# Kernel tuning notes

Hardware: AMD Instinct MI355X
Metric: run time of the kernel (lower is better)

Reference implementation:

```python
import jax, jax.numpy as jnp
import numpy as np

R = 32768          # number of human-object pairs
IN_FEATS = 3072    # input_size * 3 (person + object + union features)
HIDDEN = 1024      # input_size
NUM_CLASSES = 50   # action classes


def setup_inputs() -> dict:
    key = jax.random.key(0)
    k_x, k_w1, k_w2 = jax.random.split(key, 3)
    x = jax.random.normal(k_x, (R, IN_FEATS), dtype=jnp.float32)
    # Linear weights init: normal(std=0.01), bias 0 (as in the module)
    w1 = jax.random.normal(k_w1, (IN_FEATS, HIDDEN), dtype=jnp.float32) * 0.01
    b1 = jnp.zeros((HIDDEN,), dtype=jnp.float32)
    w2 = jax.random.normal(k_w2, (HIDDEN, NUM_CLASSES), dtype=jnp.float32) * 0.01
    b2 = jnp.zeros((NUM_CLASSES,), dtype=jnp.float32)
    return {"x": x, "w1": w1, "b1": b1, "w2": w2, "b2": b2}


def reference(x, w1, b1, w2, b2):
    # HoiOutputLayers.forward: scores = cls_score(relu(cls_fc1(x)))
    h = jax.nn.relu(jnp.dot(x, w1) + b1)          # [R, HIDDEN]
    scores = jnp.dot(h, w2) + b2                  # [R, NUM_CLASSES] action logits
    return scores
```

## Files before the change

### kernel.cpp

```cpp
#include <hip/hip_runtime.h>

#define K1 3072
#define N1 1024
#define NCOL 50

typedef float  f32x4  __attribute__((ext_vector_type(4)));
typedef short  short8 __attribute__((ext_vector_type(8)));

#define GLD16(g, l)                                                        \
  __builtin_amdgcn_global_load_lds(                                        \
      (const __attribute__((address_space(1))) void*)(g),                  \
      (__attribute__((address_space(3))) void*)(l), 16, 0, 0)

#define MFMA_BF16(a, b, c) __builtin_amdgcn_mfma_f32_16x16x32_bf16(a, b, c, 0, 0, 0)

__device__ inline unsigned bfr(float f) {
  return (__builtin_bit_cast(unsigned, f) + 0x8000u) >> 16;
}
__device__ inline short f2bf(float f) { return (short)bfr(f); }
__device__ inline short8 cvt8(float4 a, float4 b) {
  short8 r;
  r[0] = f2bf(a.x); r[1] = f2bf(a.y); r[2] = f2bf(a.z); r[3] = f2bf(a.w);
  r[4] = f2bf(b.x); r[5] = f2bf(b.y); r[6] = f2bf(b.z); r[7] = f2bf(b.w);
  return r;
}

__global__ __launch_bounds__(256) void w1t_kernel(const float* __restrict__ W1,
                                                  short* __restrict__ W1T) {
  __shared__ float tile[64 * 65];
  const int t = threadIdx.x, b = blockIdx.x;
  const int k0 = (b >> 4) * 64, n0 = (b & 15) * 64;
#pragma unroll
  for (int i = 0; i < 16; ++i) {
    const int e = t + i * 256, r = e >> 6, c = e & 63;
    tile[r * 65 + c] = W1[(size_t)(k0 + r) * N1 + n0 + c];
  }
  __syncthreads();
#pragma unroll
  for (int i = 0; i < 16; ++i) {
    const int e = t + i * 256, kx = e & 63, ny = e >> 6;
    W1T[(size_t)(n0 + ny) * K1 + k0 + kx] = f2bf(tile[kx * 65 + ny]);
  }
}

__global__ __launch_bounds__(256) void w2t_kernel(const float* __restrict__ W2,
                                                  short* __restrict__ W2T) {
  const int idx = blockIdx.x * 256 + threadIdx.x;
  for (int e = idx; e < 64 * N1; e += 16 * 256) {
    const int c = e >> 10, k = e & 1023;
    const float v = (c < NCOL) ? W2[(size_t)k * NCOL + c] : 0.f;
    W2T[(size_t)c * N1 + k] = f2bf(v);
  }
}

#define BK2 64
#define NIT (K1 / BK2)
#define ASLOT (256 * 64)
#define SH2 264

struct __align__(16) Smem2 {
  union {
    struct { short A[2][ASLOT]; short B[2][ASLOT]; } s;
    struct { short h[128 * SH2]; short w2t[64 * SH2]; } e;
  } u;
};

__global__ __launch_bounds__(512, 2)
void hoi_fused2(const float* __restrict__ X, const short* __restrict__ W1T,
                const float* __restrict__ B1, const short* __restrict__ W2T,
                const float* __restrict__ B2, float* __restrict__ OUT) {
  __shared__ Smem2 sm;
  const int tid  = threadIdx.x;
  const int lane = tid & 63, wid = tid >> 6;
  const int wr = wid >> 2, wc = wid & 3;
  const int l15 = lane & 15, g = lane >> 4, l7 = l15 & 7;

  const int bid  = blockIdx.x;
  const int gidx = (bid & 7) * 64 + (bid >> 3);
  const int m_blk = gidx >> 2, n_blk = gidx & 3;
  const int m0 = m_blk * 256, n0 = n_blk * 256;

  const int ar = tid >> 1;
  const int ah = tid & 1;
  const float* aptr = X + (size_t)(m0 + ar) * K1 + ah * 32;
  const int awr = ar * 64;
  const int ar7 = ar & 7;

  const int srow  = lane >> 3;
  const int sslot = (lane & 7) ^ srow;
  const short* bS0 = W1T + (size_t)(n0 + 0   + wid * 16 + srow) * K1 + sslot * 8;
  const short* bS1 = W1T + (size_t)(n0 + 128 + wid * 16 + srow) * K1 + sslot * 8;
  const int dL0 = (0   + wid * 16) * 64;
  const int dL1 = (128 + wid * 16) * 64;

#define ISSUE_B0(kt, sl) do { GLD16(bS0 + (size_t)(kt) * BK2,                  &sm.u.s.B[sl][dL0]);        \
                              GLD16(bS0 + (size_t)8 * K1 + (size_t)(kt) * BK2, &sm.u.s.B[sl][dL0 + 512]); } while (0)
#define ISSUE_B1(kt, sl) do { GLD16(bS1 + (size_t)(kt) * BK2,                  &sm.u.s.B[sl][dL1]);        \
                              GLD16(bS1 + (size_t)8 * K1 + (size_t)(kt) * BK2, &sm.u.s.B[sl][dL1 + 512]); } while (0)

  const int aRd = (wr * 128 + l15) * 64;
  const int bRd = (wc * 64  + l15) * 64;
  const int sk0 = ((g)     ^ l7) * 8;
  const int sk1 = ((4 | g) ^ l7) * 8;

  float b1v[4];
#pragma unroll
  for (int nf = 0; nf < 4; ++nf) b1v[nf] = B1[n0 + wc * 64 + nf * 16 + l15];

  f32x4 acc[8][4] = {};
  float4 ra[8];

  ISSUE_B0(0, 0); ISSUE_B1(0, 0);
#pragma unroll
  for (int q = 0; q < 8; ++q) ra[q] = *(const float4*)(aptr + 4 * q);
#pragma unroll
  for (int j = 0; j < 4; ++j) {
    const short8 v = cvt8(ra[2 * j], ra[2 * j + 1]);
    *(short8*)&sm.u.s.A[0][awr + (((ah << 2) | j) ^ ar7) * 8] = v;
  }
#pragma unroll
  for (int q = 0; q < 8; ++q) ra[q] = *(const float4*)(aptr + BK2 + 4 * q);

  for (int t = 0; t < NIT; ++t) {
    const int s  = t & 1, sx = s ^ 1;
    const int tn = (t + 1 < NIT) ? t + 1 : NIT - 1;
    const int ta = (t + 2 < NIT) ? t + 2 : NIT - 1;

    asm volatile("s_waitcnt vmcnt(8)" ::: "memory");
    asm volatile("s_waitcnt lgkmcnt(0)" ::: "memory");
    __builtin_amdgcn_s_barrier();
    __builtin_amdgcn_sched_barrier(0);

    short8 a_[4][2], b_[4][2];

#pragma unroll
    for (int mf = 0; mf < 4; ++mf) {
      a_[mf][0] = *(const short8*)&sm.u.s.A[s][aRd + mf * 1024 + sk0];
      a_[mf][1] = *(const short8*)&sm.u.s.A[s][aRd + mf * 1024 + sk1];
    }
#pragma unroll
    for (int nf = 0; nf < 2; ++nf) {
      b_[nf][0] = *(const short8*)&sm.u.s.B[s][bRd + nf * 1024 + sk0];
      b_[nf][1] = *(const short8*)&sm.u.s.B[s][bRd + nf * 1024 + sk1];
    }
    asm volatile("s_waitcnt lgkmcnt(0)" ::: "memory");
    __builtin_amdgcn_sched_barrier(0);
    __builtin_amdgcn_s_setprio(1);
#pragma unroll
    for (int mf = 0; mf < 4; ++mf)
#pragma unroll
      for (int nf = 0; nf < 2; ++nf) {
        acc[mf][nf] = MFMA_BF16(a_[mf][0], b_[nf][0], acc[mf][nf]);
        acc[mf][nf] = MFMA_BF16(a_[mf][1], b_[nf][1], acc[mf][nf]);
      }
    __builtin_amdgcn_s_setprio(0);
    ISSUE_B0(tn, sx);
    __builtin_amdgcn_sched_barrier(0);

#pragma unroll
    for (int nf = 2; nf < 4; ++nf) {
      b_[nf][0] = *(const short8*)&sm.u.s.B[s][bRd + nf * 1024 + sk0];
      b_[nf][1] = *(const short8*)&sm.u.s.B[s][bRd + nf * 1024 + sk1];
    }
    asm volatile("s_waitcnt lgkmcnt(0)" ::: "memory");
    __builtin_amdgcn_sched_barrier(0);
    __builtin_amdgcn_s_setprio(1);
#pragma unroll
    for (int mf = 0; mf < 4; ++mf)
#pragma unroll
      for (int nf = 2; nf < 4; ++nf) {
        acc[mf][nf] = MFMA_BF16(a_[mf][0], b_[nf][0], acc[mf][nf]);
        acc[mf][nf] = MFMA_BF16(a_[mf][1], b_[nf][1], acc[mf][nf]);
      }
    __builtin_amdgcn_s_setprio(0);
    ISSUE_B1(tn, sx);
    __builtin_amdgcn_sched_barrier(0);

#pragma unroll
    for (int mf = 0; mf < 4; ++mf) {
      a_[mf][0] = *(const short8*)&sm.u.s.A[s][aRd + (4 + mf) * 1024 + sk0];
      a_[mf][1] = *(const short8*)&sm.u.s.A[s][aRd + (4 + mf) * 1024 + sk1];
    }
    asm volatile("s_waitcnt lgkmcnt(0)" ::: "memory");
    __builtin_amdgcn_sched_barrier(0);
    __builtin_amdgcn_s_setprio(1);
#pragma unroll
    for (int mf = 0; mf < 4; ++mf)
#pragma unroll
      for (int nf = 0; nf < 2; ++nf) {
        acc[4 + mf][nf] = MFMA_BF16(a_[mf][0], b_[nf][0], acc[4 + mf][nf]);
        acc[4 + mf][nf] = MFMA_BF16(a_[mf][1], b_[nf][1], acc[4 + mf][nf]);
      }
    __builtin_amdgcn_s_setprio(0);
#pragma unroll
    for (int j = 0; j < 4; ++j) {
      const short8 v = cvt8(ra[2 * j], ra[2 * j + 1]);
      *(short8*)&sm.u.s.A[sx][awr + (((ah << 2) | j) ^ ar7) * 8] = v;
    }
    __builtin_amdgcn_sched_barrier(0);

    __builtin_amdgcn_s_setprio(1);
#pragma unroll
    for (int mf = 0; mf < 4; ++mf)
#pragma unroll
      for (int nf = 2; nf < 4; ++nf) {
        acc[4 + mf][nf] = MFMA_BF16(a_[mf][0], b_[nf][0], acc[4 + mf][nf]);
        acc[4 + mf][nf] = MFMA_BF16(a_[mf][1], b_[nf][1], acc[4 + mf][nf]);
      }
    __builtin_amdgcn_s_setprio(0);
    {
      const float* ap = aptr + (size_t)ta * BK2;
#pragma unroll
      for (int q = 0; q < 8; ++q) ra[q] = *(const float4*)(ap + 4 * q);
    }
    __builtin_amdgcn_sched_barrier(0);
  }
#undef ISSUE_B0
#undef ISSUE_B1

  for (int ph = 0; ph < 2; ++ph) {
    __syncthreads();

    if (wr == ph) {
#pragma unroll
      for (int mf = 0; mf < 8; ++mf)
#pragma unroll
        for (int nf = 0; nf < 4; ++nf) {
          const int c = wc * 64 + nf * 16 + l15;
#pragma unroll
          for (int j = 0; j < 4; ++j) {
            const int r = mf * 16 + g * 4 + j;
            sm.u.e.h[r * SH2 + c] = f2bf(fmaxf(acc[mf][nf][j] + b1v[nf], 0.f));
          }
        }
    }
    if (ph == 0) {
      const int c = tid & 63, part = tid >> 6;
#pragma unroll
      for (int i = 0; i < 4; ++i)
        *(short8*)&sm.u.e.w2t[c * SH2 + part * 32 + i * 8] =
            *(const short8*)&W2T[(size_t)c * N1 + n0 + part * 32 + i * 8];
    }
    __syncthreads();

    f32x4 acc2[4] = {};
#pragma unroll
    for (int ks = 0; ks < 8; ++ks) {
      const short8 a2 = *(const short8*)&sm.u.e.h[(wid * 16 + l15) * SH2 + ks * 32 + g * 8];
#pragma unroll
      for (int nt = 0; nt < 4; ++nt) {
        const short8 b2 = *(const short8*)&sm.u.e.w2t[(nt * 16 + l15) * SH2 + ks * 32 + g * 8];
        acc2[nt] = MFMA_BF16(a2, b2, acc2[nt]);
      }
    }
#pragma unroll
    for (int nt = 0; nt < 4; ++nt) {
      const int c = nt * 16 + l15;
      if (c < NCOL) {
#pragma unroll
        for (int j = 0; j < 4; ++j) {
          const int r = m0 + ph * 128 + wid * 16 + g * 4 + j;
          float v = acc2[nt][j];
          if (n_blk == 0) v += B2[c];
          atomicAdd(&OUT[(size_t)r * NCOL + c], v);
        }
      }
    }
  }
}

#define BK 32
#define NSTEP (K1 / BK)
#define SAS 40
#define SHS 136

struct __align__(16) Smem0 {
  union {
    struct { short A[128 * SAS]; short BT[128 * SAS]; } s[2];
    struct { short h[64 * SHS]; short w2t[64 * SHS]; } e;
  } u;
};

__global__ __launch_bounds__(256, 3)
void hoi_fused0(const float* __restrict__ X, const float* __restrict__ W1,
                const float* __restrict__ B1, const float* __restrict__ W2,
                const float* __restrict__ B2, float* __restrict__ OUT) {
  __shared__ Smem0 sm;
  const int tid  = threadIdx.x;
  const int lane = tid & 63, wid = tid >> 6;
  const int wr = wid >> 1, wc = wid & 1;
  const int l15 = lane & 15, g = lane >> 4;
  const int bid   = blockIdx.x;
  const int xcd   = bid & 7, o = bid >> 3;
  const int m_blk = xcd * 32 + (o >> 3);
  const int n_blk = o & 7;
  const int m0 = m_blk * 128, n0 = n_blk * 128;

  const int arow = tid >> 1;
  const int akc  = (tid & 1) << 4;
  const float* aptr = X + (size_t)(m0 + arow) * K1 + akc;
  const int bk2 = tid >> 4, bcm = tid & 15;
  const float* bptr = W1 + (size_t)(2 * bk2) * N1 + n0 + bcm;

  float b1v[4];
#pragma unroll
  for (int nt = 0; nt < 4; ++nt) b1v[nt] = B1[n0 + wc * 64 + nt * 16 + l15];

  f32x4 acc[4][4] = {};
  float4 ra[4];
  float  rb0[8], rb1[8];
#pragma unroll
  for (int q = 0; q < 4; ++q) ra[q] = *(const float4*)(aptr + 4 * q);
#pragma unroll
  for (int i = 0; i < 8; ++i) { rb0[i] = bptr[16 * i]; rb1[i] = bptr[N1 + 16 * i]; }

  for (int step = 0; step < NSTEP; ++step) {
    const int cb = step & 1;
    const short8 av0 = cvt8(ra[0], ra[1]);
    const short8 av1 = cvt8(ra[2], ra[3]);
    unsigned bpk[8];
#pragma unroll
    for (int i = 0; i < 8; ++i)
      bpk[i] = bfr(rb0[i]) | ((__builtin_bit_cast(unsigned, rb1[i]) + 0x8000u) & 0xFFFF0000u);
    if (step + 1 < NSTEP) {
      const int k0v = (step + 1) * BK;
#pragma unroll
      for (int q = 0; q < 4; ++q) ra[q] = *(const float4*)(aptr + k0v + 4 * q);
      const float* bp = bptr + (size_t)k0v * N1;
#pragma unroll
      for (int i = 0; i < 8; ++i) { rb0[i] = bp[16 * i]; rb1[i] = bp[N1 + 16 * i]; }
    }
    *(short8*)&sm.u.s[cb].A[arow * SAS + akc + 0] = av0;
    *(short8*)&sm.u.s[cb].A[arow * SAS + akc + 8] = av1;
#pragma unroll
    for (int i = 0; i < 8; ++i)
      *(unsigned*)&sm.u.s[cb].BT[(bcm + 16 * i) * SAS + 2 * bk2] = bpk[i];

    asm volatile("s_waitcnt lgkmcnt(0)" ::: "memory");
    __builtin_amdgcn_s_barrier();
    __builtin_amdgcn_sched_barrier(0);

    short8 af[4];
#pragma unroll
    for (int mt = 0; mt < 4; ++mt)
      af[mt] = *(const short8*)&sm.u.s[cb].A[(wr * 64 + mt * 16 + l15) * SAS + g * 8];
#pragma unroll
    for (int nt = 0; nt < 4; ++nt) {
      short8 bfv = *(const short8*)&sm.u.s[cb].BT[(wc * 64 + nt * 16 + l15) * SAS + g * 8];
#pragma unroll
      for (int mt = 0; mt < 4; ++mt)
        acc[mt][nt] = MFMA_BF16(af[mt], bfv, acc[mt][nt]);
    }
  }

  for (int p = 0; p < 2; ++p) {
    __syncthreads();
    if (wr == p) {
#pragma unroll
      for (int mt = 0; mt < 4; ++mt)
#pragma unroll
        for (int nt = 0; nt < 4; ++nt) {
          const int c = wc * 64 + nt * 16 + l15;
#pragma unroll
          for (int j = 0; j < 4; ++j) {
            const int r = mt * 16 + g * 4 + j;
            sm.u.e.h[r * SHS + c] = f2bf(fmaxf(acc[mt][nt][j] + b1v[nt], 0.f));
          }
        }
    }
    if (p == 0) {
      const int kk = tid >> 1, ch = (tid & 1) * 32;
#pragma unroll
      for (int i = 0; i < 32; ++i) {
        const int c = ch + i;
        const float v = (c < NCOL) ? W2[(size_t)kk * NCOL + c] * 0.f + ((c < NCOL) ? W2[(size_t)(n0 + kk) * NCOL + c] : 0.f) : 0.f;
        sm.u.e.w2t[c * SHS + kk] = f2bf(v);
      }
    }
    __syncthreads();

    f32x4 acc2[4] = {};
#pragma unroll
    for (int ks = 0; ks < 4; ++ks) {
      const short8 a2f = *(const short8*)&sm.u.e.h[(wid * 16 + l15) * SHS + ks * 32 + g * 8];
#pragma unroll
      for (int nt2 = 0; nt2 < 4; ++nt2) {
        const short8 b2f = *(const short8*)&sm.u.e.w2t[(nt2 * 16 + l15) * SHS + ks * 32 + g * 8];
        acc2[nt2] = MFMA_BF16(a2f, b2f, acc2[nt2]);
      }
    }
#pragma unroll
    for (int nt2 = 0; nt2 < 4; ++nt2) {
      const int c = nt2 * 16 + l15;
      if (c < NCOL) {
#pragma unroll
        for (int j = 0; j < 4; ++j) {
          const int r = m0 + p * 64 + wid * 16 + g * 4 + j;
          float v = acc2[nt2][j];
          if (n_blk == 0) v += B2[c];
          atomicAdd(&OUT[(size_t)r * NCOL + c], v);
        }
      }
    }
  }
}

extern "C" void kernel_launch(void* const* d_in, const int* in_sizes, int n_in,
                              void* d_out, int out_size, void* d_ws, size_t ws_size,
                              hipStream_t stream) {
  const float* X  = (const float*)d_in[0];
  const float* W1 = (const float*)d_in[1];
  const float* B1 = (const float*)d_in[2];
  const float* W2 = (const float*)d_in[3];
  const float* B2 = (const float*)d_in[4];
  float* OUT = (float*)d_out;

  const size_t W1T_BYTES = (size_t)N1 * K1 * 2;
  const size_t W2T_BYTES = (size_t)64 * N1 * 2;

  hipMemsetAsync(d_out, 0, (size_t)out_size * sizeof(float), stream);

  if (ws_size >= W1T_BYTES + W2T_BYTES) {
    short* W1T = (short*)d_ws;
    short* W2T = (short*)((char*)d_ws + W1T_BYTES);
    hipLaunchKernelGGL(w1t_kernel, dim3(768), dim3(256), 0, stream, W1, W1T);
    hipLaunchKernelGGL(w2t_kernel, dim3(16), dim3(256), 0, stream, W2, W2T);
    hipLaunchKernelGGL(hoi_fused2, dim3(512), dim3(512), 0, stream, X, W1T, B1, W2T, B2, OUT);
  } else {
    hipLaunchKernelGGL(hoi_fused0, dim3(2048), dim3(256), 0, stream, X, W1, B1, W2, B2, OUT);
  }
}
```

Measured before the change: 361.3 us.

## Pre-convert X to bf16 and stream A tiles via direct global-to-LDS loads

Adds a separate kernel that converts the whole fp32 input X to bf16 in workspace. The main GEMM then loads A tiles with global_load_lds, the same way as B, instead of loading fp32 through registers and converting inside the loop, and the pipeline issue and wait structure is rearranged around that. This removes conversion ALU work and register pressure from the hot loop, and it halves A traffic inside the GEMM, which rereads each X tile once per N block. The cost is an extra pass that reads X once in fp32 and writes a bf16 copy (about 200 MB of workspace), plus the requirement for a large workspace; if the workspace is too small, the fallback kernel runs instead.

```diff
diff --git a/kernel.cpp b/kernel.cpp
--- a/kernel.cpp
+++ b/kernel.cpp
@@ -23,6 +23,18 @@
   r[0] = f2bf(a.x); r[1] = f2bf(a.y); r[2] = f2bf(a.z); r[3] = f2bf(a.w);
   r[4] = f2bf(b.x); r[5] = f2bf(b.y); r[6] = f2bf(b.z); r[7] = f2bf(b.w);
   return r;
+}
+
+__global__ __launch_bounds__(512) void xcvt_kernel(const float* __restrict__ X,
+                                                   short* __restrict__ Xb) {
+  size_t i = ((size_t)blockIdx.x * 512 + threadIdx.x) * 8;
+  const size_t stride = (size_t)2048 * 512 * 8;
+#pragma unroll 4
+  for (int it = 0; it < 12; ++it, i += stride) {
+    float4 u = *(const float4*)(X + i);
+    float4 v = *(const float4*)(X + i + 4);
+    *(short8*)(Xb + i) = cvt8(u, v);
+  }
 }
 
 __global__ __launch_bounds__(256) void w1t_kernel(const float* __restrict__ W1,
@@ -66,7 +78,7 @@
 };
 
 __global__ __launch_bounds__(512, 2)
-void hoi_fused2(const float* __restrict__ X, const short* __restrict__ W1T,
+void hoi_fused2(const short* __restrict__ Xb, const short* __restrict__ W1T,
                 const float* __restrict__ B1, const short* __restrict__ W2T,
                 const float* __restrict__ B2, float* __restrict__ OUT) {
   __shared__ Smem2 sm;
@@ -80,19 +92,19 @@
   const int m_blk = gidx >> 2, n_blk = gidx & 3;
   const int m0 = m_blk * 256, n0 = n_blk * 256;
 
-  const int ar = tid >> 1;
-  const int ah = tid & 1;
-  const float* aptr = X + (size_t)(m0 + ar) * K1 + ah * 32;
-  const int awr = ar * 64;
-  const int ar7 = ar & 7;
-
   const int srow  = lane >> 3;
   const int sslot = (lane & 7) ^ srow;
+  const short* aS0 = Xb  + (size_t)(m0 + 0   + wid * 16 + srow) * K1 + sslot * 8;
+  const short* aS1 = Xb  + (size_t)(m0 + 128 + wid * 16 + srow) * K1 + sslot * 8;
   const short* bS0 = W1T + (size_t)(n0 + 0   + wid * 16 + srow) * K1 + sslot * 8;
   const short* bS1 = W1T + (size_t)(n0 + 128 + wid * 16 + srow) * K1 + sslot * 8;
   const int dL0 = (0   + wid * 16) * 64;
   const int dL1 = (128 + wid * 16) * 64;
 
+#define ISSUE_A0(kt, sl) do { GLD16(aS0 + (size_t)(kt) * BK2,                  &sm.u.s.A[sl][dL0]);        \
+                              GLD16(aS0 + (size_t)8 * K1 + (size_t)(kt) * BK2, &sm.u.s.A[sl][dL0 + 512]); } while (0)
+#define ISSUE_A1(kt, sl) do { GLD16(aS1 + (size_t)(kt) * BK2,                  &sm.u.s.A[sl][dL1]);        \
+                              GLD16(aS1 + (size_t)8 * K1 + (size_t)(kt) * BK2, &sm.u.s.A[sl][dL1 + 512]); } while (0)
 #define ISSUE_B0(kt, sl) do { GLD16(bS0 + (size_t)(kt) * BK2,                  &sm.u.s.B[sl][dL0]);        \
                               GLD16(bS0 + (size_t)8 * K1 + (size_t)(kt) * BK2, &sm.u.s.B[sl][dL0 + 512]); } while (0)
 #define ISSUE_B1(kt, sl) do { GLD16(bS1 + (size_t)(kt) * BK2,                  &sm.u.s.B[sl][dL1]);        \
@@ -108,27 +120,22 @@
   for (int nf = 0; nf < 4; ++nf) b1v[nf] = B1[n0 + wc * 64 + nf * 16 + l15];
 
   f32x4 acc[8][4] = {};
-  float4 ra[8];
-
-  ISSUE_B0(0, 0); ISSUE_B1(0, 0);
-#pragma unroll
-  for (int q = 0; q < 8; ++q) ra[q] = *(const float4*)(aptr + 4 * q);
-#pragma unroll
-  for (int j = 0; j < 4; ++j) {
-    const short8 v = cvt8(ra[2 * j], ra[2 * j + 1]);
-    *(short8*)&sm.u.s.A[0][awr + (((ah << 2) | j) ^ ar7) * 8] = v;
-  }
-#pragma unroll
-  for (int q = 0; q < 8; ++q) ra[q] = *(const float4*)(aptr + BK2 + 4 * q);
+
+  ISSUE_A0(0, 0); ISSUE_A1(0, 0); ISSUE_B0(0, 0); ISSUE_B1(0, 0);
 
   for (int t = 0; t < NIT; ++t) {
     const int s  = t & 1, sx = s ^ 1;
     const int tn = (t + 1 < NIT) ? t + 1 : NIT - 1;
-    const int ta = (t + 2 < NIT) ? t + 2 : NIT - 1;
-
-    asm volatile("s_waitcnt vmcnt(8)" ::: "memory");
-    asm volatile("s_waitcnt lgkmcnt(0)" ::: "memory");
+
     __builtin_amdgcn_s_barrier();
+    ISSUE_A0(tn, sx);
+    __builtin_amdgcn_sched_barrier(0);
+    asm volatile("s_waitcnt vmcnt(2)" ::: "memory");
+    __builtin_amdgcn_s_barrier();
+    __builtin_amdgcn_sched_barrier(0);
+    ISSUE_A1(tn, sx);
+    ISSUE_B0(tn, sx);
+    ISSUE_B1(tn, sx);
     __builtin_amdgcn_sched_barrier(0);
 
     short8 a_[4][2], b_[4][2];
@@ -154,7 +161,6 @@
         acc[mf][nf] = MFMA_BF16(a_[mf][1], b_[nf][1], acc[mf][nf]);
       }
     __builtin_amdgcn_s_setprio(0);
-    ISSUE_B0(tn, sx);
     __builtin_amdgcn_sched_barrier(0);
 
 #pragma unroll
@@ -173,7 +179,6 @@
         acc[mf][nf] = MFMA_BF16(a_[mf][1], b_[nf][1], acc[mf][nf]);
       }
     __builtin_amdgcn_s_setprio(0);
-    ISSUE_B1(tn, sx);
     __builtin_amdgcn_sched_barrier(0);
 
 #pragma unroll
@@ -192,11 +197,6 @@
         acc[4 + mf][nf] = MFMA_BF16(a_[mf][1], b_[nf][1], acc[4 + mf][nf]);
       }
     __builtin_amdgcn_s_setprio(0);
-#pragma unroll
-    for (int j = 0; j < 4; ++j) {
-      const short8 v = cvt8(ra[2 * j], ra[2 * j + 1]);
-      *(short8*)&sm.u.s.A[sx][awr + (((ah << 2) | j) ^ ar7) * 8] = v;
-    }
     __builtin_amdgcn_sched_barrier(0);
 
     __builtin_amdgcn_s_setprio(1);
@@ -208,13 +208,9 @@
         acc[4 + mf][nf] = MFMA_BF16(a_[mf][1], b_[nf][1], acc[4 + mf][nf]);
       }
     __builtin_amdgcn_s_setprio(0);
-    {
-      const float* ap = aptr + (size_t)ta * BK2;
-#pragma unroll
-      for (int q = 0; q < 8; ++q) ra[q] = *(const float4*)(ap + 4 * q);
-    }
-    __builtin_amdgcn_sched_barrier(0);
-  }
+  }
+#undef ISSUE_A0
+#undef ISSUE_A1
 #undef ISSUE_B0
 #undef ISSUE_B1
 
@@ -373,7 +369,7 @@
 #pragma unroll
       for (int i = 0; i < 32; ++i) {
         const int c = ch + i;
-        const float v = (c < NCOL) ? W2[(size_t)kk * NCOL + c] * 0.f + ((c < NCOL) ? W2[(size_t)(n0 + kk) * NCOL + c] : 0.f) : 0.f;
+        const float v = (c < NCOL) ? W2[(size_t)(n0 + kk) * NCOL + c] : 0.f;
         sm.u.e.w2t[c * SHS + kk] = f2bf(v);
       }
     }
@@ -415,17 +411,20 @@
   const float* B2 = (const float*)d_in[4];
   float* OUT = (float*)d_out;
 
+  const size_t XB_BYTES  = (size_t)32768 * K1 * 2;
   const size_t W1T_BYTES = (size_t)N1 * K1 * 2;
   const size_t W2T_BYTES = (size_t)64 * N1 * 2;
 
   hipMemsetAsync(d_out, 0, (size_t)out_size * sizeof(float), stream);
 
-  if (ws_size >= W1T_BYTES + W2T_BYTES) {
-    short* W1T = (short*)d_ws;
-    short* W2T = (short*)((char*)d_ws + W1T_BYTES);
+  if (ws_size >= XB_BYTES + W1T_BYTES + W2T_BYTES) {
+    short* Xb  = (short*)d_ws;
+    short* W1T = (short*)((char*)d_ws + XB_BYTES);
+    short* W2T = (short*)((char*)d_ws + XB_BYTES + W1T_BYTES);
+    hipLaunchKernelGGL(xcvt_kernel, dim3(2048), dim3(512), 0, stream, X, Xb);
     hipLaunchKernelGGL(w1t_kernel, dim3(768), dim3(256), 0, stream, W1, W1T);
     hipLaunchKernelGGL(w2t_kernel, dim3(16), dim3(256), 0, stream, W2, W2T);
-    hipLaunchKernelGGL(hoi_fused2, dim3(512), dim3(512), 0, stream, X, W1T, B1, W2T, B2, OUT);
+    hipLaunchKernelGGL(hoi_fused2, dim3(512), dim3(512), 0, stream, Xb, W1T, B1, W2T, B2, OUT);
   } else {
     hipLaunchKernelGGL(hoi_fused0, dim3(2048), dim3(256), 0, stream, X, W1, B1, W2, B2, OUT);
   }
```

New measurement: 340.4 us. -5.8%, faster.

## Restructure main GEMM loop: issue all prefetches at top, batch LDS reads

Applied to the files above, without the earlier changes.

Rewrites the per-iteration schedule of the first GEMM. The A-tile convert/store, both W1 global-to-LDS loads and the next X prefetch are now issued at the start of each iteration, followed by all LDS fragment reads, with partial lgkmcnt waits between MFMA groups. The old schedule interleaved prefetches between MFMA phases. The aim is fewer LDS waits and fuller MFMA issue, but it adds an extra barrier per iteration, more live registers from the second A fragment set, and a full vmcnt(0) wait that exposes global load latency. It also removes a redundant dead W2 load in the epilogue.

```diff
diff --git a/kernel.cpp b/kernel.cpp
--- a/kernel.cpp
+++ b/kernel.cpp
@@ -80,8 +80,8 @@
   const int m_blk = gidx >> 2, n_blk = gidx & 3;
   const int m0 = m_blk * 256, n0 = n_blk * 256;
 
-  const int ar = tid >> 1;
-  const int ah = tid & 1;
+  const int ar  = tid >> 1;
+  const int ah  = tid & 1;
   const float* aptr = X + (size_t)(m0 + ar) * K1 + ah * 32;
   const int awr = ar * 64;
   const int ar7 = ar & 7;
@@ -110,9 +110,10 @@
   f32x4 acc[8][4] = {};
   float4 ra[8];
 
+#pragma unroll
+  for (int q = 0; q < 8; ++q) ra[q] = *(const float4*)(aptr + 4 * q);
   ISSUE_B0(0, 0); ISSUE_B1(0, 0);
-#pragma unroll
-  for (int q = 0; q < 8; ++q) ra[q] = *(const float4*)(aptr + 4 * q);
+  asm volatile("s_waitcnt vmcnt(4)" ::: "memory");
 #pragma unroll
   for (int j = 0; j < 4; ++j) {
     const short8 v = cvt8(ra[2 * j], ra[2 * j + 1]);
@@ -120,18 +121,38 @@
   }
 #pragma unroll
   for (int q = 0; q < 8; ++q) ra[q] = *(const float4*)(aptr + BK2 + 4 * q);
+  asm volatile("s_waitcnt lgkmcnt(0)" ::: "memory");
+  __builtin_amdgcn_s_barrier();
 
   for (int t = 0; t < NIT; ++t) {
     const int s  = t & 1, sx = s ^ 1;
     const int tn = (t + 1 < NIT) ? t + 1 : NIT - 1;
     const int ta = (t + 2 < NIT) ? t + 2 : NIT - 1;
 
-    asm volatile("s_waitcnt vmcnt(8)" ::: "memory");
+    asm volatile("s_waitcnt vmcnt(0)" ::: "memory");
+    __builtin_amdgcn_sched_barrier(0);
+    short8 av[4];
+#pragma unroll
+    for (int j = 0; j < 4; ++j) av[j] = cvt8(ra[2 * j], ra[2 * j + 1]);
+    __builtin_amdgcn_sched_barrier(0);
+
+    __builtin_amdgcn_s_barrier();
+#pragma unroll
+    for (int j = 0; j < 4; ++j)
+      *(short8*)&sm.u.s.A[sx][awr + (((ah << 2) | j) ^ ar7) * 8] = av[j];
+    ISSUE_B0(tn, sx);
+    ISSUE_B1(tn, sx);
+    {
+      const float* ap = aptr + (size_t)ta * BK2;
+#pragma unroll
+      for (int q = 0; q < 8; ++q) ra[q] = *(const float4*)(ap + 4 * q);
+    }
+    __builtin_amdgcn_sched_barrier(0);
     asm volatile("s_waitcnt lgkmcnt(0)" ::: "memory");
     __builtin_amdgcn_s_barrier();
     __builtin_amdgcn_sched_barrier(0);
 
-    short8 a_[4][2], b_[4][2];
+    short8 a_[4][2], b_[4][2], a2_[4][2];
 
 #pragma unroll
     for (int mf = 0; mf < 4; ++mf) {
@@ -143,7 +164,21 @@
       b_[nf][0] = *(const short8*)&sm.u.s.B[s][bRd + nf * 1024 + sk0];
       b_[nf][1] = *(const short8*)&sm.u.s.B[s][bRd + nf * 1024 + sk1];
     }
-    asm volatile("s_waitcnt lgkmcnt(0)" ::: "memory");
+    __builtin_amdgcn_sched_barrier(0);
+#pragma unroll
+    for (int nf = 2; nf < 4; ++nf) {
+      b_[nf][0] = *(const short8*)&sm.u.s.B[s][bRd + nf * 1024 + sk0];
+      b_[nf][1] = *(const short8*)&sm.u.s.B[s][bRd + nf * 1024 + sk1];
+    }
+    __builtin_amdgcn_sched_barrier(0);
+#pragma unroll
+    for (int mf = 0; mf < 4; ++mf) {
+      a2_[mf][0] = *(const short8*)&sm.u.s.A[s][aRd + (4 + mf) * 1024 + sk0];
+      a2_[mf][1] = *(const short8*)&sm.u.s.A[s][aRd + (4 + mf) * 1024 + sk1];
+    }
+    __builtin_amdgcn_sched_barrier(0);
+
+    asm volatile("s_waitcnt lgkmcnt(12)" ::: "memory");
     __builtin_amdgcn_sched_barrier(0);
     __builtin_amdgcn_s_setprio(1);
 #pragma unroll
@@ -154,15 +189,9 @@
         acc[mf][nf] = MFMA_BF16(a_[mf][1], b_[nf][1], acc[mf][nf]);
       }
     __builtin_amdgcn_s_setprio(0);
-    ISSUE_B0(tn, sx);
-    __builtin_amdgcn_sched_barrier(0);
-
-#pragma unroll
-    for (int nf = 2; nf < 4; ++nf) {
-      b_[nf][0] = *(const short8*)&sm.u.s.B[s][bRd + nf * 1024 + sk0];
-      b_[nf][1] = *(const short8*)&sm.u.s.B[s][bRd + nf * 1024 + sk1];
-    }
-    asm volatile("s_waitcnt lgkmcnt(0)" ::: "memory");
+    __builtin_amdgcn_sched_barrier(0);
+
+    asm volatile("s_waitcnt lgkmcnt(8)" ::: "memory");
     __builtin_amdgcn_sched_barrier(0);
     __builtin_amdgcn_s_setprio(1);
 #pragma unroll
@@ -173,14 +202,8 @@
         acc[mf][nf] = MFMA_BF16(a_[mf][1], b_[nf][1], acc[mf][nf]);
       }
     __builtin_amdgcn_s_setprio(0);
-    ISSUE_B1(tn, sx);
-    __builtin_amdgcn_sched_barrier(0);
-
-#pragma unroll
-    for (int mf = 0; mf < 4; ++mf) {
-      a_[mf][0] = *(const short8*)&sm.u.s.A[s][aRd + (4 + mf) * 1024 + sk0];
-      a_[mf][1] = *(const short8*)&sm.u.s.A[s][aRd + (4 + mf) * 1024 + sk1];
-    }
+    __builtin_amdgcn_sched_barrier(0);
+
     asm volatile("s_waitcnt lgkmcnt(0)" ::: "memory");
     __builtin_amdgcn_sched_barrier(0);
     __builtin_amdgcn_s_setprio(1);
@@ -188,32 +211,17 @@
     for (int mf = 0; mf < 4; ++mf)
 #pragma unroll
       for (int nf = 0; nf < 2; ++nf) {
-        acc[4 + mf][nf] = MFMA_BF16(a_[mf][0], b_[nf][0], acc[4 + mf][nf]);
-        acc[4 + mf][nf] = MFMA_BF16(a_[mf][1], b_[nf][1], acc[4 + mf][nf]);
+        acc[4 + mf][nf] = MFMA_BF16(a2_[mf][0], b_[nf][0], acc[4 + mf][nf]);
+        acc[4 + mf][nf] = MFMA_BF16(a2_[mf][1], b_[nf][1], acc[4 + mf][nf]);
+      }
+#pragma unroll
+    for (int mf = 0; mf < 4; ++mf)
+#pragma unroll
+      for (int nf = 2; nf < 4; ++nf) {
+        acc[4 + mf][nf] = MFMA_BF16(a2_[mf][0], b_[nf][0], acc[4 + mf][nf]);
+        acc[4 + mf][nf] = MFMA_BF16(a2_[mf][1], b_[nf][1], acc[4 + mf][nf]);
       }
     __builtin_amdgcn_s_setprio(0);
-#pragma unroll
-    for (int j = 0; j < 4; ++j) {
-      const short8 v = cvt8(ra[2 * j], ra[2 * j + 1]);
-      *(short8*)&sm.u.s.A[sx][awr + (((ah << 2) | j) ^ ar7) * 8] = v;
-    }
-    __builtin_amdgcn_sched_barrier(0);
-
-    __builtin_amdgcn_s_setprio(1);
-#pragma unroll
-    for (int mf = 0; mf < 4; ++mf)
-#pragma unroll
-      for (int nf = 2; nf < 4; ++nf) {
-        acc[4 + mf][nf] = MFMA_BF16(a_[mf][0], b_[nf][0], acc[4 + mf][nf]);
-        acc[4 + mf][nf] = MFMA_BF16(a_[mf][1], b_[nf][1], acc[4 + mf][nf]);
-      }
-    __builtin_amdgcn_s_setprio(0);
-    {
-      const float* ap = aptr + (size_t)ta * BK2;
-#pragma unroll
-      for (int q = 0; q < 8; ++q) ra[q] = *(const float4*)(ap + 4 * q);
-    }
-    __builtin_amdgcn_sched_barrier(0);
   }
 #undef ISSUE_B0
 #undef ISSUE_B1
@@ -373,7 +381,7 @@
 #pragma unroll
       for (int i = 0; i < 32; ++i) {
         const int c = ch + i;
-        const float v = (c < NCOL) ? W2[(size_t)kk * NCOL + c] * 0.f + ((c < NCOL) ? W2[(size_t)(n0 + kk) * NCOL + c] : 0.f) : 0.f;
+        const float v = (c < NCOL) ? W2[(size_t)(n0 + kk) * NCOL + c] : 0.f;
         sm.u.e.w2t[c * SHS + kk] = f2bf(v);
       }
     }
```

New measurement: 617.9 us. +71.0%, slower.
